# Optimization experiments

Measured on AMD Instinct MI355X. Metric: run time of the kernel, lower is better.

## Reference

```python
import jax, jax.numpy as jnp
import numpy as np

N = 10000      # nodes
E = 160000     # edges
B = 16         # graphs in batch
F_NODE = 42
F_EDGE = 12
D = 256        # hidden_dim
H = 4          # heads
C = D // H     # per-head channels = 64
L = 5          # num_layers
NEG_SLOPE = 0.2  # GATConv leaky_relu slope


def layernorm(x, g, b, eps=1e-5):
    mu = jnp.mean(x, axis=-1, keepdims=True)
    var = jnp.var(x, axis=-1, keepdims=True)
    return (x - mu) * jax.lax.rsqrt(var + eps) * g + b


def setup_inputs() -> dict:
    key = jax.random.key(0)
    ks = jax.random.split(key, 20)
    def w(i, shape, scale=0.05):
        return jax.random.normal(ks[i], shape, dtype=jnp.float32) * scale
    return {
        "x": jax.random.normal(ks[0], (N, F_NODE), dtype=jnp.float32),
        "edge_attr": jax.random.normal(ks[1], (E, F_EDGE), dtype=jnp.float32),
        "edge_index": jax.random.randint(ks[2], (2, E), 0, N),
        "batch": jnp.sort(jax.random.randint(ks[3], (N,), 0, B)),
        # node / edge encoders
        "enc_w": w(4, (F_NODE, D)), "enc_b": jnp.zeros((D,), jnp.float32),
        "eenc_w": w(5, (F_EDGE, D)), "eenc_b": jnp.zeros((D,), jnp.float32),
        # stacked GAT layer params [L, ...]
        "gat_w": w(6, (L, D, D)),          # lin_src == lin_dst (shared in PyG for Tensor input)
        "att_src": w(7, (L, H, C)),
        "att_dst": w(8, (L, H, C)),
        "att_edge": w(9, (L, H, C)),
        "gat_ew": w(10, (L, D, D)),        # lin_edge
        "gat_b": jnp.zeros((L, D), jnp.float32),
        "ln_g": jnp.ones((L, D), jnp.float32),
        "ln_b": jnp.zeros((L, D), jnp.float32),
        # attention pooling gate MLP
        "gate_w1": w(11, (D, D)), "gate_b1": jnp.zeros((D,), jnp.float32),
        "gate_w2": w(12, (D, 1)), "gate_b2": jnp.zeros((1,), jnp.float32),
        # MLP readout (mlp_layers=2)
        "ro_w1": w(13, (D, D)), "ro_b1": jnp.zeros((D,), jnp.float32),
        "ro_w2": w(14, (D, D)), "ro_b2": jnp.zeros((D,), jnp.float32),
    }


def reference(x, edge_index, edge_attr, batch, enc_w, enc_b, eenc_w, eenc_b,
              gat_w, att_src, att_dst, att_edge, gat_ew, gat_b, ln_g, ln_b,
              gate_w1, gate_b1, gate_w2, gate_b2, ro_w1, ro_b1, ro_w2, ro_b2):
    src0, dst0 = edge_index[0], edge_index[1]

    # encoders (dropout is identity at eval)
    h = jax.nn.relu(x @ enc_w + enc_b)                      # [N, D]
    e = jax.nn.relu(edge_attr @ eenc_w + eenc_b)            # [E, D]

    # GATConv add_self_loops with fill_value='mean': self-loop edge feature is
    # the mean of incoming edge features per destination node.
    esum = jax.ops.segment_sum(e, dst0, num_segments=N)
    cnt = jax.ops.segment_sum(jnp.ones((E,), e.dtype), dst0, num_segments=N)
    e_self = esum / jnp.maximum(cnt, 1.0)[:, None]
    e_full = jnp.concatenate([e, e_self], axis=0)           # [E+N, D]
    loops = jnp.arange(N)
    src = jnp.concatenate([src0, loops])
    dst = jnp.concatenate([dst0, loops])

    for l in range(L):
        xh = (h @ gat_w[l]).reshape(N, H, C)                # [N, H, C]
        a_s = jnp.einsum('nhc,hc->nh', xh, att_src[l])      # [N, H]
        a_d = jnp.einsum('nhc,hc->nh', xh, att_dst[l])
        eh = (e_full @ gat_ew[l]).reshape(-1, H, C)         # [E+N, H, C]
        a_e = jnp.einsum('ehc,hc->eh', eh, att_edge[l])
        alpha = jax.nn.leaky_relu(a_s[src] + a_d[dst] + a_e, NEG_SLOPE)  # [E+N, H]
        # softmax over incoming edges per destination node (stable)
        m = jax.lax.stop_gradient(jax.ops.segment_max(alpha, dst, num_segments=N))
        ex = jnp.exp(alpha - m[dst])
        den = jax.ops.segment_sum(ex, dst, num_segments=N)
        attn = ex / den[dst]                                # [E+N, H]
        msg = xh[src] * attn[:, :, None]                    # [E+N, H, C]
        out = jax.ops.segment_sum(msg, dst, num_segments=N).reshape(N, D) + gat_b[l]
        out = jax.nn.relu(layernorm(out, ln_g[l], ln_b[l]))
        h = h + out                                         # residual

    # GlobalAttention pooling: softmax(gate_nn(h)) per graph, weighted sum
    gate = (jax.nn.relu(h @ gate_w1 + gate_b1) @ gate_w2 + gate_b2)[:, 0]  # [N]
    gm = jax.lax.stop_gradient(jax.ops.segment_max(gate, batch, num_segments=B))
    ge = jnp.exp(gate - gm[batch])
    gd = jax.ops.segment_sum(ge, batch, num_segments=B)
    wgt = ge / gd[batch]
    g_embed = jax.ops.segment_sum(h * wgt[:, None], batch, num_segments=B)  # [B, D]

    # MLP readout
    return jax.nn.relu(g_embed @ ro_w1 + ro_b1) @ ro_w2 + ro_b2  # [B, D]
```

## Files before the change

### kernel.cpp

```cpp
#include <hip/hip_runtime.h>
#include <math.h>

#define DD 256
#define HH 4
#define CC 64
#define LL 5
#define NEG_SLOPE 0.2f
#define LH 20
#define WCAP 192

typedef __bf16 bf16x8 __attribute__((ext_vector_type(8)));
typedef __bf16 bf16x4 __attribute__((ext_vector_type(4)));
typedef float f32x4 __attribute__((ext_vector_type(4)));

static __device__ __forceinline__ float lrelu(float x) {
    return x > 0.0f ? x : NEG_SLOPE * x;
}

__global__ __launch_bounds__(256) void wproj_kernel(
    const float* __restrict__ gat_ew, const float* __restrict__ att_edge,
    float* __restrict__ wproj) {
    int l = blockIdx.x;
    int k = threadIdx.x;
    const float* W = gat_ew + (size_t)l * DD * DD;
    const float* att = att_edge + l * DD;
    for (int hh = 0; hh < HH; ++hh) {
        float s = 0.f;
        #pragma unroll
        for (int c = 0; c < CC; ++c)
            s += W[k * DD + hh * CC + c] * att[hh * CC + c];
        wproj[k * LH + l * HH + hh] = s;
    }
}

__global__ __launch_bounds__(256) void pack_edge_frags_kernel(
    const float* __restrict__ eenc_w, const float* __restrict__ eenc_b,
    const float* __restrict__ wproj, __bf16* __restrict__ wfe,
    __bf16* __restrict__ wfp) {
    int tid = threadIdx.x;
    for (int idx = tid; idx < 16 * 64; idx += 256) {
        int t = idx >> 6, lane = idx & 63;
        int q = lane >> 4, r15 = lane & 15;
        int col = t * 16 + r15;
        #pragma unroll
        for (int j = 0; j < 8; ++j) {
            int k = q * 8 + j;
            float v = (k < 12) ? eenc_w[k * 256 + col]
                               : (k == 12 ? eenc_b[col] : 0.f);
            wfe[(size_t)idx * 8 + j] = (__bf16)v;
        }
    }
    for (int idx = tid; idx < 16 * 64; idx += 256) {
        int sidx = idx >> 6, lane = idx & 63;
        int s = sidx >> 1, t2 = sidx & 1;
        int q = lane >> 4, r15 = lane & 15;
        int col = t2 * 16 + r15;
        #pragma unroll
        for (int j = 0; j < 8; ++j) {
            int k = s * 32 + q * 8 + j;
            float v = (col < LH) ? wproj[k * LH + col] : 0.f;
            wfp[(size_t)idx * 8 + j] = (__bf16)v;
        }
    }
}

__global__ __launch_bounds__(256) void wswizzle_kernel(
    const float* __restrict__ gat_w, const float* __restrict__ gate_w1,
    __bf16* __restrict__ wf) {
    int b = blockIdx.x;
    int l = b >> 5;
    int rem = b & 31;
    int y = rem >> 3, ks = rem & 7;
    int tid = threadIdx.x;
    int t = tid >> 6, lane = tid & 63;
    int q = lane >> 4, r15 = lane & 15;
    const float* W = (l < 5) ? (gat_w + (size_t)l * DD * DD) : gate_w1;
    size_t obase = (((size_t)b * 4 + t) * 64 + lane) * 8;
    int kbase = ks * 32 + q * 8;
    int col = y * 64 + t * 16 + r15;
    #pragma unroll
    for (int j = 0; j < 8; ++j)
        wf[obase + j] = (__bf16)W[(size_t)(kbase + j) * DD + col];
}

__global__ __launch_bounds__(256) void encoder_kernel(
    const float* __restrict__ x, const float* __restrict__ enc_w,
    const float* __restrict__ enc_b, float* __restrict__ h,
    __bf16* __restrict__ hbf, int N) {
    int n = blockIdx.x;
    int tid = threadIdx.x;
    __shared__ float xs[42];
    if (tid < 42) xs[tid] = x[(size_t)n * 42 + tid];
    __syncthreads();
    float acc = enc_b[tid];
    #pragma unroll
    for (int f = 0; f < 42; ++f) acc += xs[f] * enc_w[f * DD + tid];
    float v = fmaxf(acc, 0.f);
    h[(size_t)n * DD + tid] = v;
    hbf[(size_t)n * DD + tid] = (__bf16)v;
}

__global__ __launch_bounds__(256) void edge_mfma_kernel(
    const float* __restrict__ edge_attr, const __bf16* __restrict__ wfe,
    const __bf16* __restrict__ wfp, const int* __restrict__ pos,
    float* __restrict__ a_e_csr, int E) {
    __shared__ __bf16 sm[4][16][264];
    int tid = threadIdx.x;
    int w = tid >> 6, lane = tid & 63;
    int q = lane >> 4, r15 = lane & 15;
    int eb = blockIdx.x * 64 + w * 16;
    int e = eb + r15;
    int ec = min(e, E - 1);
    bf16x8 a1;
    #pragma unroll
    for (int j = 0; j < 8; ++j) a1[j] = (__bf16)0.f;
    if (q == 0) {
        const float4* p = (const float4*)(edge_attr + (size_t)ec * 12);
        float4 p0 = p[0], p1 = p[1];
        a1[0] = (__bf16)p0.x; a1[1] = (__bf16)p0.y; a1[2] = (__bf16)p0.z; a1[3] = (__bf16)p0.w;
        a1[4] = (__bf16)p1.x; a1[5] = (__bf16)p1.y; a1[6] = (__bf16)p1.z; a1[7] = (__bf16)p1.w;
    } else if (q == 1) {
        float4 p2 = *(const float4*)(edge_attr + (size_t)ec * 12 + 8);
        a1[0] = (__bf16)p2.x; a1[1] = (__bf16)p2.y; a1[2] = (__bf16)p2.z; a1[3] = (__bf16)p2.w;
        a1[4] = (__bf16)1.0f;
    }
    const bf16x8* wfeP = (const bf16x8*)wfe;
    f32x4 zero = (f32x4){0.f, 0.f, 0.f, 0.f};
    #pragma unroll
    for (int t = 0; t < 16; ++t) {
        bf16x8 bfr = wfeP[t * 64 + lane];
        f32x4 c = __builtin_amdgcn_mfma_f32_16x16x32_bf16(a1, bfr, zero, 0, 0, 0);
        int col = t * 16 + r15;
        #pragma unroll
        for (int r = 0; r < 4; ++r)
            sm[w][q * 4 + r][col] = (__bf16)fmaxf(c[r], 0.f);
    }
    const bf16x8* wfpP = (const bf16x8*)wfp;
    f32x4 c2[2];
    c2[0] = zero; c2[1] = zero;
    #pragma unroll
    for (int s = 0; s < 8; ++s) {
        bf16x8 a2 = *(const bf16x8*)&sm[w][r15][s * 32 + q * 8];
        #pragma unroll
        for (int t2 = 0; t2 < 2; ++t2)
            c2[t2] = __builtin_amdgcn_mfma_f32_16x16x32_bf16(
                a2, wfpP[(s * 2 + t2) * 64 + lane], c2[t2], 0, 0, 0);
    }
    #pragma unroll
    for (int t2 = 0; t2 < 2; ++t2) {
        int col = t2 * 16 + r15;
        if (col >= LH) continue;
        #pragma unroll
        for (int r = 0; r < 4; ++r) {
            int e2 = eb + q * 4 + r;
            if (e2 < E) {
                int pk = pos[e2];
                a_e_csr[(size_t)pk * LH + col] = c2[t2][r];
            }
        }
    }
}

__global__ void deg_kernel(const int* __restrict__ dst, int* __restrict__ deg, int E) {
    int e = blockIdx.x * 256 + threadIdx.x;
    if (e < E) atomicAdd(&deg[dst[e]], 1);
}

__global__ void self_ae_kernel(const int* __restrict__ row_ptr,
                               float* __restrict__ a_e_csr, int N, int E) {
    int i = blockIdx.x * 256 + threadIdx.x;
    if (i >= N * LH) return;
    int n = i / LH;
    int j = i % LH;
    int rs = row_ptr[n], re = row_ptr[n + 1];
    float s = 0.f;
    for (int k = rs; k < re; ++k)
        s += a_e_csr[(size_t)k * LH + j];
    a_e_csr[(size_t)(E + n) * LH + j] = s / (float)max(re - rs, 1);
}

__global__ __launch_bounds__(1024) void scan_kernel(const int* __restrict__ deg,
                                                    int* __restrict__ row_ptr,
                                                    int* __restrict__ cursor, int n) {
    __shared__ int wsum[16];
    __shared__ int carry_s;
    int tid = threadIdx.x;
    int w = tid >> 6, lane = tid & 63;
    if (tid == 0) carry_s = 0;
    __syncthreads();
    for (int base = 0; base < n; base += 1024) {
        int i = base + tid;
        int v = (i < n) ? deg[i] : 0;
        int carry = carry_s;
        int s = v;
        #pragma unroll
        for (int off = 1; off < 64; off <<= 1) {
            int t = __shfl_up(s, off, 64);
            if (lane >= off) s += t;
        }
        if (lane == 63) wsum[w] = s;
        __syncthreads();
        if (w == 0 && lane < 16) {
            int ws = wsum[lane];
            #pragma unroll
            for (int off = 1; off < 16; off <<= 1) {
                int t = __shfl_up(ws, off, 64);
                if (lane >= off) ws += t;
            }
            wsum[lane] = ws;
        }
        __syncthreads();
        int waveoff = (w == 0) ? 0 : wsum[w - 1];
        if (i < n) {
            int ex = carry + waveoff + s - v;
            row_ptr[i] = ex;
            cursor[i] = ex;
        }
        __syncthreads();
        if (tid == 0) carry_s = carry + wsum[15];
        __syncthreads();
    }
    if (tid == 0) row_ptr[n] = carry_s;
}

__global__ void scatter_kernel(const int* __restrict__ src, const int* __restrict__ dst,
                               int* __restrict__ cursor, int* __restrict__ csr_src,
                               int* __restrict__ pos, int E) {
    int e = blockIdx.x * 256 + threadIdx.x;
    if (e >= E) return;
    int d = dst[e];
    int pk = atomicAdd(&cursor[d], 1);
    csr_src[pk] = src[e];
    pos[e] = pk;
}

__global__ __launch_bounds__(256) void gemm_mfma_kernel(
    const __bf16* __restrict__ hbf, const __bf16* __restrict__ wf,
    __bf16* __restrict__ xhbf, int M,
    const float* __restrict__ att_src, const float* __restrict__ att_dst,
    float* __restrict__ a_s, float* __restrict__ a_d,
    const float* __restrict__ bias, const float* __restrict__ gate_w2,
    const float* __restrict__ gate_b2, float* __restrict__ gate_out) {
    int tid = threadIdx.x;
    int w = tid >> 6, lane = tid & 63;
    int q = lane >> 4, r15 = lane & 15;
    int m0 = blockIdx.x * 64;
    int y = blockIdx.y;
    int arow = m0 + w * 16 + r15;
    int arowc = min(arow, M - 1);
    const __bf16* ap = hbf + (size_t)arowc * DD + q * 8;
    const bf16x8* bp0 = (const bf16x8*)wf + (size_t)(y * 8) * 4 * 64 + lane;
    f32x4 acc[4];
    #pragma unroll
    for (int t = 0; t < 4; ++t) acc[t] = (f32x4){0.f, 0.f, 0.f, 0.f};
    #pragma unroll
    for (int ks = 0; ks < 8; ++ks) {
        bf16x8 a = *(const bf16x8*)(ap + ks * 32);
        const bf16x8* bp = bp0 + (size_t)ks * 4 * 64;
        #pragma unroll
        for (int t = 0; t < 4; ++t) {
            bf16x8 b = bp[(size_t)t * 64];
            acc[t] = __builtin_amdgcn_mfma_f32_16x16x32_bf16(a, b, acc[t], 0, 0, 0);
        }
    }
    if (xhbf) {
        #pragma unroll
        for (int t = 0; t < 4; ++t) {
            int col = y * 64 + t * 16 + r15;
            #pragma unroll
            for (int r = 0; r < 4; ++r) {
                int rc = m0 + w * 16 + q * 4 + r;
                if (rc < M) xhbf[(size_t)rc * DD + col] = (__bf16)acc[t][r];
            }
        }
    }
    if (att_src) {
        #pragma unroll
        for (int r = 0; r < 4; ++r) {
            float ps = 0.f, pd = 0.f;
            #pragma unroll
            for (int t = 0; t < 4; ++t) {
                int col = y * 64 + t * 16 + r15;
                ps += acc[t][r] * att_src[col];
                pd += acc[t][r] * att_dst[col];
            }
            #pragma unroll
            for (int mask = 1; mask < 16; mask <<= 1) {
                ps += __shfl_xor(ps, mask, 64);
                pd += __shfl_xor(pd, mask, 64);
            }
            int rc = m0 + w * 16 + q * 4 + r;
            if (r15 == 0 && rc < M) {
                a_s[rc * HH + y] = ps;
                a_d[rc * HH + y] = pd;
            }
        }
    }
    if (gate_w2) {
        #pragma unroll
        for (int r = 0; r < 4; ++r) {
            float pg = 0.f;
            #pragma unroll
            for (int t = 0; t < 4; ++t) {
                int col = y * 64 + t * 16 + r15;
                pg += fmaxf(acc[t][r] + bias[col], 0.f) * gate_w2[col];
            }
            #pragma unroll
            for (int mask = 1; mask < 16; mask <<= 1) pg += __shfl_xor(pg, mask, 64);
            int rc = m0 + w * 16 + q * 4 + r;
            if (r15 == 0 && rc < M) {
                float add = pg + (y == 0 ? gate_b2[0] : 0.f);
                atomicAdd(&gate_out[rc], add);
            }
        }
    }
}

__global__ __launch_bounds__(256) void gat_message6_kernel(
    const __bf16* __restrict__ xhbf, const float* __restrict__ a_s,
    const float* __restrict__ a_d, const float* __restrict__ a_e,
    const int* __restrict__ row_ptr, const int* __restrict__ csr_src,
    const float* __restrict__ gat_b,
    const float* __restrict__ ln_g, const float* __restrict__ ln_b,
    float* __restrict__ h, __bf16* __restrict__ hbf, int N, int E) {
    __shared__ float lws[4][WCAP * 4];
    int tid = threadIdx.x;
    int w = tid >> 6, lane = tid & 63;
    int n = blockIdx.x * 4 + w;
    if (n >= N) return;
    int hh = lane >> 4, j = lane & 15;
    int rs = row_ptr[n], re = row_ptr[n + 1];
    int deg = re - rs;
    float adn = a_d[n * HH + hh];
    float al_self = lrelu(a_s[n * HH + hh] + adn + a_e[(size_t)(E + n) * LH + hh]);
    float m = al_self, den = 0.f;
    for (int k = rs + j; k < re; k += 16) {
        int kk = k - rs;
        int s = csr_src[k];
        float a = lrelu(a_s[s * HH + hh] + adn + a_e[(size_t)k * LH + hh]);
        if (kk < WCAP) lws[w][kk * 4 + hh] = a;
        float mn = fmaxf(m, a);
        den = den * __expf(m - mn) + __expf(a - mn);
        m = mn;
    }
    #pragma unroll
    for (int off = 1; off < 16; off <<= 1) {
        float m2 = __shfl_xor(m, off, 64);
        float d2 = __shfl_xor(den, off, 64);
        float mn = fmaxf(m, m2);
        den = den * __expf(m - mn) + d2 * __expf(m2 - mn);
        m = mn;
    }
    den += __expf(al_self - m);
    float inv_den = 1.0f / den;
    int cap = min(deg, WCAP);
    for (int kk = j; kk < cap; kk += 16)
        lws[w][kk * 4 + hh] = __expf(lws[w][kk * 4 + hh] - m) * inv_den;
    float wself = __expf(al_self - m) * inv_den;
    bf16x4 xsb = *((const bf16x4*)(xhbf + (size_t)n * DD) + lane);
    float4 acc;
    acc.x = wself * (float)xsb[0]; acc.y = wself * (float)xsb[1];
    acc.z = wself * (float)xsb[2]; acc.w = wself * (float)xsb[3];
    int k = rs;
    for (; k + 1 < re; k += 2) {
        int kk0 = k - rs, kk1 = kk0 + 1;
        int s0 = csr_src[k], s1_ = csr_src[k + 1];
        float w0, w1;
        if (kk0 < WCAP) w0 = lws[w][kk0 * 4 + hh];
        else w0 = __expf(lrelu(a_s[s0 * HH + hh] + adn + a_e[(size_t)k * LH + hh]) - m) * inv_den;
        if (kk1 < WCAP) w1 = lws[w][kk1 * 4 + hh];
        else w1 = __expf(lrelu(a_s[s1_ * HH + hh] + adn + a_e[(size_t)(k + 1) * LH + hh]) - m) * inv_den;
        bf16x4 x0 = *((const bf16x4*)(xhbf + (size_t)s0 * DD) + lane);
        bf16x4 x1 = *((const bf16x4*)(xhbf + (size_t)s1_ * DD) + lane);
        acc.x += w0 * (float)x0[0] + w1 * (float)x1[0];
        acc.y += w0 * (float)x0[1] + w1 * (float)x1[1];
        acc.z += w0 * (float)x0[2] + w1 * (float)x1[2];
        acc.w += w0 * (float)x0[3] + w1 * (float)x1[3];
    }
    if (k < re) {
        int kk0 = k - rs;
        int s0 = csr_src[k];
        float w0;
        if (kk0 < WCAP) w0 = lws[w][kk0 * 4 + hh];
        else w0 = __expf(lrelu(a_s[s0 * HH + hh] + adn + a_e[(size_t)k * LH + hh]) - m) * inv_den;
        bf16x4 x0 = *((const bf16x4*)(xhbf + (size_t)s0 * DD) + lane);
        acc.x += w0 * (float)x0[0]; acc.y += w0 * (float)x0[1];
        acc.z += w0 * (float)x0[2]; acc.w += w0 * (float)x0[3];
    }
    float4 gb = *((const float4*)gat_b + lane);
    float4 val;
    val.x = acc.x + gb.x; val.y = acc.y + gb.y;
    val.z = acc.z + gb.z; val.w = acc.w + gb.w;
    float s1 = val.x + val.y + val.z + val.w;
    float s2 = val.x * val.x + val.y * val.y + val.z * val.z + val.w * val.w;
    #pragma unroll
    for (int off = 1; off < 64; off <<= 1) {
        s1 += __shfl_xor(s1, off, 64);
        s2 += __shfl_xor(s2, off, 64);
    }
    float mu = s1 * (1.0f / DD);
    float var = s2 * (1.0f / DD) - mu * mu;
    float rstd = rsqrtf(var + 1e-5f);
    float4 lg = *((const float4*)ln_g + lane);
    float4 lb = *((const float4*)ln_b + lane);
    float4 nv;
    nv.x = fmaxf((val.x - mu) * rstd * lg.x + lb.x, 0.f);
    nv.y = fmaxf((val.y - mu) * rstd * lg.y + lb.y, 0.f);
    nv.z = fmaxf((val.z - mu) * rstd * lg.z + lb.z, 0.f);
    nv.w = fmaxf((val.w - mu) * rstd * lg.w + lb.w, 0.f);
    float4* hp = (float4*)(h + (size_t)n * DD) + lane;
    float4 hv = *hp;
    hv.x += nv.x; hv.y += nv.y; hv.z += nv.z; hv.w += nv.w;
    *hp = hv;
    bf16x4 hb;
    hb[0] = (__bf16)hv.x; hb[1] = (__bf16)hv.y;
    hb[2] = (__bf16)hv.z; hb[3] = (__bf16)hv.w;
    *((bf16x4*)(hbf + (size_t)n * DD) + lane) = hb;
}

__global__ void bstart_kernel(const int* __restrict__ batch, int* __restrict__ bstart,
                              int N, int B) {
    int b = threadIdx.x;
    if (b > B) return;
    int lo = 0, hi = N;
    while (lo < hi) {
        int mid = (lo + hi) >> 1;
        if (batch[mid] < b) lo = mid + 1; else hi = mid;
    }
    bstart[b] = lo;
}

__global__ __launch_bounds__(256) void gseg_kernel(
    const float* __restrict__ gate, const int* __restrict__ bstart,
    float* __restrict__ gmax, float* __restrict__ gden) {
    int b = blockIdx.x;
    int tid = threadIdx.x;
    int s0 = bstart[b], s1 = bstart[b + 1];
    __shared__ float red[256];
    float m = -1e30f;
    for (int i = s0 + tid; i < s1; i += 256) m = fmaxf(m, gate[i]);
    red[tid] = m;
    __syncthreads();
    for (int off = 128; off; off >>= 1) {
        if (tid < off) red[tid] = fmaxf(red[tid], red[tid + off]);
        __syncthreads();
    }
    float gm = red[0];
    __syncthreads();
    float s = 0.f;
    for (int i = s0 + tid; i < s1; i += 256) s += __expf(gate[i] - gm);
    red[tid] = s;
    __syncthreads();
    for (int off = 128; off; off >>= 1) {
        if (tid < off) red[tid] += red[tid + off];
        __syncthreads();
    }
    if (tid == 0) {
        gmax[b] = gm;
        gden[b] = red[0];
    }
}

#define POOL_CHUNK 32
__global__ __launch_bounds__(256) void pool_scatter_kernel(
    const float* __restrict__ h, const float* __restrict__ gate,
    const float* __restrict__ gmax, const float* __restrict__ gden,
    const int* __restrict__ batch, float* __restrict__ g_embed, int N) {
    int i0 = blockIdx.x * POOL_CHUNK;
    int d = threadIdx.x;
    int iend = min(i0 + POOL_CHUNK, N);
    float acc = 0.f;
    int cur = batch[i0];
    for (int i = i0; i < iend; ++i) {
        int b = batch[i];
        if (b != cur) {
            atomicAdd(&g_embed[cur * DD + d], acc);
            acc = 0.f;
            cur = b;
        }
        float wgt = __expf(gate[i] - gmax[b]) / gden[b];
        acc += wgt * h[(size_t)i * DD + d];
    }
    atomicAdd(&g_embed[cur * DD + d], acc);
}

__global__ __launch_bounds__(256) void readout_kernel(
    const float* __restrict__ g_embed, const float* __restrict__ w1,
    const float* __restrict__ b1, const float* __restrict__ w2,
    const float* __restrict__ b2, float* __restrict__ out) {
    int b = blockIdx.x;
    int tid = threadIdx.x;
    __shared__ float gvec[256];
    __shared__ float hid[256];
    gvec[tid] = g_embed[b * DD + tid];
    __syncthreads();
    float hv = b1[tid];
    for (int k = 0; k < DD; ++k) hv += gvec[k] * w1[k * DD + tid];
    hid[tid] = fmaxf(hv, 0.f);
    __syncthreads();
    float o = b2[tid];
    for (int t = 0; t < DD; ++t) o += hid[t] * w2[t * DD + tid];
    out[b * DD + tid] = o;
}

extern "C" void kernel_launch(void* const* d_in, const int* in_sizes, int n_in,
                              void* d_out, int out_size, void* d_ws, size_t ws_size,
                              hipStream_t stream) {
    const float* x        = (const float*)d_in[0];
    const float* edge_attr= (const float*)d_in[1];
    const int*   edge_idx = (const int*)d_in[2];
    const int*   batch    = (const int*)d_in[3];
    const float* enc_w    = (const float*)d_in[4];
    const float* enc_b    = (const float*)d_in[5];
    const float* eenc_w   = (const float*)d_in[6];
    const float* eenc_b   = (const float*)d_in[7];
    const float* gat_w    = (const float*)d_in[8];
    const float* att_src  = (const float*)d_in[9];
    const float* att_dst  = (const float*)d_in[10];
    const float* att_edge = (const float*)d_in[11];
    const float* gat_ew   = (const float*)d_in[12];
    const float* gat_b    = (const float*)d_in[13];
    const float* ln_g     = (const float*)d_in[14];
    const float* ln_b     = (const float*)d_in[15];
    const float* gate_w1  = (const float*)d_in[16];
    const float* gate_b1  = (const float*)d_in[17];
    const float* gate_w2  = (const float*)d_in[18];
    const float* gate_b2  = (const float*)d_in[19];
    const float* ro_w1    = (const float*)d_in[20];
    const float* ro_b1    = (const float*)d_in[21];
    const float* ro_w2    = (const float*)d_in[22];
    const float* ro_b2    = (const float*)d_in[23];
    float* out = (float*)d_out;

    const int N = in_sizes[0] / 42;
    const int E = in_sizes[1] / 12;
    const int B = out_size / DD;

    char* p = (char*)d_ws;
    auto alloc = [&](size_t bytes) {
        char* r = p;
        p += (bytes + 255) & ~(size_t)255;
        return (void*)r;
    };
    float*  h       = (float*)alloc((size_t)N * DD * 4);
    __bf16* hbf     = (__bf16*)alloc((size_t)N * DD * 2);
    __bf16* xhbf    = (__bf16*)alloc((size_t)N * DD * 2);
    float*  a_s     = (float*)alloc((size_t)N * HH * 4);
    float*  a_d     = (float*)alloc((size_t)N * HH * 4);
    float*  a_e_csr = (float*)alloc((size_t)(E + N) * LH * 4);
    float*  wproj   = (float*)alloc((size_t)DD * LH * 4);
    __bf16* wfe     = (__bf16*)alloc((size_t)16 * 64 * 8 * 2);
    __bf16* wfp     = (__bf16*)alloc((size_t)16 * 64 * 8 * 2);
    __bf16* wf      = (__bf16*)alloc((size_t)6 * DD * DD * 2);
    float*  gate    = (float*)alloc((size_t)N * 4);
    float*  g_embed = (float*)alloc((size_t)B * DD * 4);
    float*  gmax    = (float*)alloc((size_t)B * 4);
    float*  gden    = (float*)alloc((size_t)B * 4);
    int* deg        = (int*)alloc((size_t)N * 4);
    int* row_ptr    = (int*)alloc((size_t)(N + 1) * 4);
    int* cursor     = (int*)alloc((size_t)N * 4);
    int* csr_src    = (int*)alloc((size_t)E * 4);
    int* pos        = (int*)alloc((size_t)E * 4);
    int* bstart     = (int*)alloc((size_t)(B + 1) * 4);

    const int* src_arr = edge_idx;
    const int* dst_arr = edge_idx + E;

    hipMemsetAsync(deg, 0, (size_t)N * 4, stream);
    hipMemsetAsync(g_embed, 0, (size_t)B * DD * 4, stream);
    hipMemsetAsync(gate, 0, (size_t)N * 4, stream);

    wproj_kernel<<<LL, 256, 0, stream>>>(gat_ew, att_edge, wproj);
    pack_edge_frags_kernel<<<1, 256, 0, stream>>>(eenc_w, eenc_b, wproj, wfe, wfp);
    wswizzle_kernel<<<192, 256, 0, stream>>>(gat_w, gate_w1, wf);
    encoder_kernel<<<N, 256, 0, stream>>>(x, enc_w, enc_b, h, hbf, N);
    deg_kernel<<<(E + 255) / 256, 256, 0, stream>>>(dst_arr, deg, E);
    scan_kernel<<<1, 1024, 0, stream>>>(deg, row_ptr, cursor, N);
    scatter_kernel<<<(E + 255) / 256, 256, 0, stream>>>(
        src_arr, dst_arr, cursor, csr_src, pos, E);
    edge_mfma_kernel<<<(E + 63) / 64, 256, 0, stream>>>(
        edge_attr, wfe, wfp, pos, a_e_csr, E);
    self_ae_kernel<<<(N * LH + 255) / 256, 256, 0, stream>>>(
        row_ptr, a_e_csr, N, E);

    dim3 ggrid((N + 63) / 64, 4);
    for (int l = 0; l < LL; ++l) {
        gemm_mfma_kernel<<<ggrid, 256, 0, stream>>>(
            hbf, wf + (size_t)l * DD * DD, xhbf, N,
            att_src + l * DD, att_dst + l * DD, a_s, a_d,
            nullptr, nullptr, nullptr, nullptr);
        gat_message6_kernel<<<(N + 3) / 4, 256, 0, stream>>>(
            xhbf, a_s, a_d, a_e_csr + l * HH, row_ptr, csr_src,
            gat_b + l * DD, ln_g + l * DD, ln_b + l * DD, h, hbf, N, E);
    }

    gemm_mfma_kernel<<<ggrid, 256, 0, stream>>>(
        hbf, wf + (size_t)5 * DD * DD, nullptr, N,
        nullptr, nullptr, nullptr, nullptr,
        gate_b1, gate_w2, gate_b2, gate);
    bstart_kernel<<<1, 32, 0, stream>>>(batch, bstart, N, B);
    gseg_kernel<<<B, 256, 0, stream>>>(gate, bstart, gmax, gden);
    pool_scatter_kernel<<<(N + POOL_CHUNK - 1) / POOL_CHUNK, 256, 0, stream>>>(
        h, gate, gmax, gden, batch, g_embed, N);
    readout_kernel<<<B, 256, 0, stream>>>(g_embed, ro_w1, ro_b1, ro_w2, ro_b2, out);
}
```

Before: 438.3 us.

## Fuse setup kernels, widen GEMM column tile, cache edge sources in LDS

Merges the wproj and edge-fragment packing kernels into one single-block kernel, and folds the batch-boundary search into the graph segment kernel, removing two launches. The node GEMM now computes 128 output columns per block with eight accumulators, halving the grid and reusing each A load across two heads. The message kernel stores each edge's source index in shared memory during the softmax pass, so the aggregation pass avoids re-reading csr_src from global memory. In exchange, the setup work is serialized in one block, and the GEMM uses more registers, which may lower occupancy.

Measured after the change: 457.9 us. 4.5% more time.

```diff
diff --git a/kernel.cpp b/kernel.cpp
--- a/kernel.cpp
+++ b/kernel.cpp
@@ -17,36 +17,34 @@
     return x > 0.0f ? x : NEG_SLOPE * x;
 }
 
-__global__ __launch_bounds__(256) void wproj_kernel(
+__global__ __launch_bounds__(256) void edge_setup_kernel(
     const float* __restrict__ gat_ew, const float* __restrict__ att_edge,
-    float* __restrict__ wproj) {
-    int l = blockIdx.x;
-    int k = threadIdx.x;
-    const float* W = gat_ew + (size_t)l * DD * DD;
-    const float* att = att_edge + l * DD;
-    for (int hh = 0; hh < HH; ++hh) {
-        float s = 0.f;
-        #pragma unroll
-        for (int c = 0; c < CC; ++c)
-            s += W[k * DD + hh * CC + c] * att[hh * CC + c];
-        wproj[k * LH + l * HH + hh] = s;
-    }
-}
-
-__global__ __launch_bounds__(256) void pack_edge_frags_kernel(
     const float* __restrict__ eenc_w, const float* __restrict__ eenc_b,
-    const float* __restrict__ wproj, __bf16* __restrict__ wfe,
+    float* __restrict__ wproj, __bf16* __restrict__ wfe,
     __bf16* __restrict__ wfp) {
     int tid = threadIdx.x;
+    int k = tid;
+    for (int l = 0; l < LL; ++l) {
+        const float* W = gat_ew + (size_t)l * DD * DD;
+        const float* att = att_edge + l * DD;
+        for (int hh = 0; hh < HH; ++hh) {
+            float s = 0.f;
+            #pragma unroll
+            for (int c = 0; c < CC; ++c)
+                s += W[k * DD + hh * CC + c] * att[hh * CC + c];
+            wproj[k * LH + l * HH + hh] = s;
+        }
+    }
+    __syncthreads();
     for (int idx = tid; idx < 16 * 64; idx += 256) {
         int t = idx >> 6, lane = idx & 63;
         int q = lane >> 4, r15 = lane & 15;
         int col = t * 16 + r15;
         #pragma unroll
         for (int j = 0; j < 8; ++j) {
-            int k = q * 8 + j;
-            float v = (k < 12) ? eenc_w[k * 256 + col]
-                               : (k == 12 ? eenc_b[col] : 0.f);
+            int kk = q * 8 + j;
+            float v = (kk < 12) ? eenc_w[kk * 256 + col]
+                                : (kk == 12 ? eenc_b[col] : 0.f);
             wfe[(size_t)idx * 8 + j] = (__bf16)v;
         }
     }
@@ -57,8 +55,8 @@
         int col = t2 * 16 + r15;
         #pragma unroll
         for (int j = 0; j < 8; ++j) {
-            int k = s * 32 + q * 8 + j;
-            float v = (col < LH) ? wproj[k * LH + col] : 0.f;
+            int kk = s * 32 + q * 8 + j;
+            float v = (col < LH) ? wproj[kk * LH + col] : 0.f;
             wfp[(size_t)idx * 8 + j] = (__bf16)v;
         }
     }
@@ -245,54 +243,60 @@
     int w = tid >> 6, lane = tid & 63;
     int q = lane >> 4, r15 = lane & 15;
     int m0 = blockIdx.x * 64;
-    int y = blockIdx.y;
+    int y2 = blockIdx.y;
     int arow = m0 + w * 16 + r15;
     int arowc = min(arow, M - 1);
     const __bf16* ap = hbf + (size_t)arowc * DD + q * 8;
-    const bf16x8* bp0 = (const bf16x8*)wf + (size_t)(y * 8) * 4 * 64 + lane;
-    f32x4 acc[4];
-    #pragma unroll
-    for (int t = 0; t < 4; ++t) acc[t] = (f32x4){0.f, 0.f, 0.f, 0.f};
+    const bf16x8* wfP = (const bf16x8*)wf;
+    f32x4 acc[8];
+    #pragma unroll
+    for (int g = 0; g < 8; ++g) acc[g] = (f32x4){0.f, 0.f, 0.f, 0.f};
     #pragma unroll
     for (int ks = 0; ks < 8; ++ks) {
         bf16x8 a = *(const bf16x8*)(ap + ks * 32);
-        const bf16x8* bp = bp0 + (size_t)ks * 4 * 64;
-        #pragma unroll
-        for (int t = 0; t < 4; ++t) {
-            bf16x8 b = bp[(size_t)t * 64];
-            acc[t] = __builtin_amdgcn_mfma_f32_16x16x32_bf16(a, b, acc[t], 0, 0, 0);
+        #pragma unroll
+        for (int g = 0; g < 8; ++g) {
+            int y = y2 * 2 + (g >> 2);
+            int t = g & 3;
+            bf16x8 b = wfP[(size_t)(((y * 8 + ks) * 4) + t) * 64 + lane];
+            acc[g] = __builtin_amdgcn_mfma_f32_16x16x32_bf16(a, b, acc[g], 0, 0, 0);
         }
     }
     if (xhbf) {
         #pragma unroll
-        for (int t = 0; t < 4; ++t) {
-            int col = y * 64 + t * 16 + r15;
+        for (int g = 0; g < 8; ++g) {
+            int col = (y2 * 8 + g) * 16 + r15;
             #pragma unroll
             for (int r = 0; r < 4; ++r) {
                 int rc = m0 + w * 16 + q * 4 + r;
-                if (rc < M) xhbf[(size_t)rc * DD + col] = (__bf16)acc[t][r];
+                if (rc < M) xhbf[(size_t)rc * DD + col] = (__bf16)acc[g][r];
             }
         }
     }
     if (att_src) {
         #pragma unroll
         for (int r = 0; r < 4; ++r) {
-            float ps = 0.f, pd = 0.f;
+            float ps0 = 0.f, pd0 = 0.f, ps1 = 0.f, pd1 = 0.f;
             #pragma unroll
-            for (int t = 0; t < 4; ++t) {
-                int col = y * 64 + t * 16 + r15;
-                ps += acc[t][r] * att_src[col];
-                pd += acc[t][r] * att_dst[col];
+            for (int g = 0; g < 8; ++g) {
+                int col = (y2 * 8 + g) * 16 + r15;
+                float v = acc[g][r];
+                if (g < 4) { ps0 += v * att_src[col]; pd0 += v * att_dst[col]; }
+                else       { ps1 += v * att_src[col]; pd1 += v * att_dst[col]; }
             }
             #pragma unroll
             for (int mask = 1; mask < 16; mask <<= 1) {
-                ps += __shfl_xor(ps, mask, 64);
-                pd += __shfl_xor(pd, mask, 64);
+                ps0 += __shfl_xor(ps0, mask, 64);
+                pd0 += __shfl_xor(pd0, mask, 64);
+                ps1 += __shfl_xor(ps1, mask, 64);
+                pd1 += __shfl_xor(pd1, mask, 64);
             }
             int rc = m0 + w * 16 + q * 4 + r;
             if (r15 == 0 && rc < M) {
-                a_s[rc * HH + y] = ps;
-                a_d[rc * HH + y] = pd;
+                a_s[rc * HH + y2 * 2 + 0] = ps0;
+                a_d[rc * HH + y2 * 2 + 0] = pd0;
+                a_s[rc * HH + y2 * 2 + 1] = ps1;
+                a_d[rc * HH + y2 * 2 + 1] = pd1;
             }
         }
     }
@@ -301,22 +305,22 @@
         for (int r = 0; r < 4; ++r) {
             float pg = 0.f;
             #pragma unroll
-            for (int t = 0; t < 4; ++t) {
-                int col = y * 64 + t * 16 + r15;
-                pg += fmaxf(acc[t][r] + bias[col], 0.f) * gate_w2[col];
+            for (int g = 0; g < 8; ++g) {
+                int col = (y2 * 8 + g) * 16 + r15;
+                pg += fmaxf(acc[g][r] + bias[col], 0.f) * gate_w2[col];
             }
             #pragma unroll
             for (int mask = 1; mask < 16; mask <<= 1) pg += __shfl_xor(pg, mask, 64);
             int rc = m0 + w * 16 + q * 4 + r;
             if (r15 == 0 && rc < M) {
-                float add = pg + (y == 0 ? gate_b2[0] : 0.f);
+                float add = pg + (y2 == 0 ? gate_b2[0] : 0.f);
                 atomicAdd(&gate_out[rc], add);
             }
         }
     }
 }
 
-__global__ __launch_bounds__(256) void gat_message6_kernel(
+__global__ __launch_bounds__(256) void gat_message7_kernel(
     const __bf16* __restrict__ xhbf, const float* __restrict__ a_s,
     const float* __restrict__ a_d, const float* __restrict__ a_e,
     const int* __restrict__ row_ptr, const int* __restrict__ csr_src,
@@ -324,6 +328,7 @@
     const float* __restrict__ ln_g, const float* __restrict__ ln_b,
     float* __restrict__ h, __bf16* __restrict__ hbf, int N, int E) {
     __shared__ float lws[4][WCAP * 4];
+    __shared__ int lsrc[4][WCAP];
     int tid = threadIdx.x;
     int w = tid >> 6, lane = tid & 63;
     int n = blockIdx.x * 4 + w;
@@ -338,7 +343,10 @@
         int kk = k - rs;
         int s = csr_src[k];
         float a = lrelu(a_s[s * HH + hh] + adn + a_e[(size_t)k * LH + hh]);
-        if (kk < WCAP) lws[w][kk * 4 + hh] = a;
+        if (kk < WCAP) {
+            lws[w][kk * 4 + hh] = a;
+            if (hh == 0) lsrc[w][kk] = s;
+        }
         float mn = fmaxf(m, a);
         den = den * __expf(m - mn) + __expf(a - mn);
         m = mn;
@@ -364,12 +372,17 @@
     int k = rs;
     for (; k + 1 < re; k += 2) {
         int kk0 = k - rs, kk1 = kk0 + 1;
-        int s0 = csr_src[k], s1_ = csr_src[k + 1];
+        int s0, s1_;
         float w0, w1;
-        if (kk0 < WCAP) w0 = lws[w][kk0 * 4 + hh];
-        else w0 = __expf(lrelu(a_s[s0 * HH + hh] + adn + a_e[(size_t)k * LH + hh]) - m) * inv_den;
-        if (kk1 < WCAP) w1 = lws[w][kk1 * 4 + hh];
-        else w1 = __expf(lrelu(a_s[s1_ * HH + hh] + adn + a_e[(size_t)(k + 1) * LH + hh]) - m) * inv_den;
+        if (kk1 < WCAP) {
+            s0 = lsrc[w][kk0]; s1_ = lsrc[w][kk1];
+            w0 = lws[w][kk0 * 4 + hh]; w1 = lws[w][kk1 * 4 + hh];
+        } else {
+            s0 = csr_src[k]; s1_ = csr_src[k + 1];
+            w0 = (kk0 < WCAP) ? lws[w][kk0 * 4 + hh]
+               : __expf(lrelu(a_s[s0 * HH + hh] + adn + a_e[(size_t)k * LH + hh]) - m) * inv_den;
+            w1 = __expf(lrelu(a_s[s1_ * HH + hh] + adn + a_e[(size_t)(k + 1) * LH + hh]) - m) * inv_den;
+        }
         bf16x4 x0 = *((const bf16x4*)(xhbf + (size_t)s0 * DD) + lane);
         bf16x4 x1 = *((const bf16x4*)(xhbf + (size_t)s1_ * DD) + lane);
         acc.x += w0 * (float)x0[0] + w1 * (float)x1[0];
@@ -379,10 +392,13 @@
     }
     if (k < re) {
         int kk0 = k - rs;
-        int s0 = csr_src[k];
+        int s0;
         float w0;
-        if (kk0 < WCAP) w0 = lws[w][kk0 * 4 + hh];
-        else w0 = __expf(lrelu(a_s[s0 * HH + hh] + adn + a_e[(size_t)k * LH + hh]) - m) * inv_den;
+        if (kk0 < WCAP) { s0 = lsrc[w][kk0]; w0 = lws[w][kk0 * 4 + hh]; }
+        else {
+            s0 = csr_src[k];
+            w0 = __expf(lrelu(a_s[s0 * HH + hh] + adn + a_e[(size_t)k * LH + hh]) - m) * inv_den;
+        }
         bf16x4 x0 = *((const bf16x4*)(xhbf + (size_t)s0 * DD) + lane);
         acc.x += w0 * (float)x0[0]; acc.y += w0 * (float)x0[1];
         acc.z += w0 * (float)x0[2]; acc.w += w0 * (float)x0[3];
@@ -418,24 +434,23 @@
     *((bf16x4*)(hbf + (size_t)n * DD) + lane) = hb;
 }
 
-__global__ void bstart_kernel(const int* __restrict__ batch, int* __restrict__ bstart,
-                              int N, int B) {
-    int b = threadIdx.x;
-    if (b > B) return;
-    int lo = 0, hi = N;
-    while (lo < hi) {
-        int mid = (lo + hi) >> 1;
-        if (batch[mid] < b) lo = mid + 1; else hi = mid;
-    }
-    bstart[b] = lo;
-}
-
 __global__ __launch_bounds__(256) void gseg_kernel(
-    const float* __restrict__ gate, const int* __restrict__ bstart,
-    float* __restrict__ gmax, float* __restrict__ gden) {
+    const float* __restrict__ gate, const int* __restrict__ batch,
+    float* __restrict__ gmax, float* __restrict__ gden, int N) {
     int b = blockIdx.x;
     int tid = threadIdx.x;
-    int s0 = bstart[b], s1 = bstart[b + 1];
+    __shared__ int bounds[2];
+    if (tid < 2) {
+        int target = b + tid;
+        int lo = 0, hi = N;
+        while (lo < hi) {
+            int mid = (lo + hi) >> 1;
+            if (batch[mid] < target) lo = mid + 1; else hi = mid;
+        }
+        bounds[tid] = lo;
+    }
+    __syncthreads();
+    int s0 = bounds[0], s1 = bounds[1];
     __shared__ float red[256];
     float m = -1e30f;
     for (int i = s0 + tid; i < s1; i += 256) m = fmaxf(m, gate[i]);
@@ -561,7 +576,6 @@
     int* cursor     = (int*)alloc((size_t)N * 4);
     int* csr_src    = (int*)alloc((size_t)E * 4);
     int* pos        = (int*)alloc((size_t)E * 4);
-    int* bstart     = (int*)alloc((size_t)(B + 1) * 4);
 
     const int* src_arr = edge_idx;
     const int* dst_arr = edge_idx + E;
@@ -570,8 +584,8 @@
     hipMemsetAsync(g_embed, 0, (size_t)B * DD * 4, stream);
     hipMemsetAsync(gate, 0, (size_t)N * 4, stream);
 
-    wproj_kernel<<<LL, 256, 0, stream>>>(gat_ew, att_edge, wproj);
-    pack_edge_frags_kernel<<<1, 256, 0, stream>>>(eenc_w, eenc_b, wproj, wfe, wfp);
+    edge_setup_kernel<<<1, 256, 0, stream>>>(gat_ew, att_edge, eenc_w, eenc_b,
+                                             wproj, wfe, wfp);
     wswizzle_kernel<<<192, 256, 0, stream>>>(gat_w, gate_w1, wf);
     encoder_kernel<<<N, 256, 0, stream>>>(x, enc_w, enc_b, h, hbf, N);
     deg_kernel<<<(E + 255) / 256, 256, 0, stream>>>(dst_arr, deg, E);
@@ -583,13 +597,13 @@
     self_ae_kernel<<<(N * LH + 255) / 256, 256, 0, stream>>>(
         row_ptr, a_e_csr, N, E);
 
-    dim3 ggrid((N + 63) / 64, 4);
+    dim3 ggrid((N + 63) / 64, 2);
     for (int l = 0; l < LL; ++l) {
         gemm_mfma_kernel<<<ggrid, 256, 0, stream>>>(
             hbf, wf + (size_t)l * DD * DD, xhbf, N,
             att_src + l * DD, att_dst + l * DD, a_s, a_d,
             nullptr, nullptr, nullptr, nullptr);
-        gat_message6_kernel<<<(N + 3) / 4, 256, 0, stream>>>(
+        gat_message7_kernel<<<(N + 3) / 4, 256, 0, stream>>>(
             xhbf, a_s, a_d, a_e_csr + l * HH, row_ptr, csr_src,
             gat_b + l * DD, ln_g + l * DD, ln_b + l * DD, h, hbf, N, E);
     }
@@ -598,8 +612,7 @@
         hbf, wf + (size_t)5 * DD * DD, nullptr, N,
         nullptr, nullptr, nullptr, nullptr,
         gate_b1, gate_w2, gate_b2, gate);
-    bstart_kernel<<<1, 32, 0, stream>>>(batch, bstart, N, B);
-    gseg_kernel<<<B, 256, 0, stream>>>(gate, bstart, gmax, gden);
+    gseg_kernel<<<B, 256, 0, stream>>>(gate, batch, gmax, gden, N);
     pool_scatter_kernel<<<(N + POOL_CHUNK - 1) / POOL_CHUNK, 256, 0, stream>>>(
         h, gate, gmax, gden, batch, g_embed, N);
     readout_kernel<<<B, 256, 0, stream>>>(g_embed, ro_w1, ro_b1, ro_w2, ro_b2, out);
```
